# Optimization experiments

Hardware: AMD Instinct MI355X
Metric: run time of the kernel (lower is better)

## Reference

```python
import jax, jax.numpy as jnp
import numpy as np
from jax import lax

HID = 768          # hidden_dim / embedding_dim
IN = 64            # input_dim = max_seq_length // num_heads
SEQ = 512          # max_seq_length
GROUPS = IN        # conv groups
BLUR_K = 5
BLUR_SIGMA = 1.0


def _gauss1d(k, sigma):
    half = (k - 1) * 0.5
    x = np.linspace(-half, half, k)
    pdf = np.exp(-0.5 * (x / sigma) ** 2)
    return pdf / pdf.sum()


def setup_inputs() -> dict:
    key = jax.random.key(0)
    ks = jax.random.split(key, 8)
    s = 0.02
    return {
        "inputs": jax.random.normal(ks[0], (16, SEQ, HID), jnp.float32),
        # Conv1d(768, 768, k=3, groups=64): weight [out_ch, in_ch/groups, k]
        "conv_w": jax.random.normal(ks[1], (HID, HID // GROUPS, 3), jnp.float32) * s,
        "conv_b": jnp.zeros((HID,), jnp.float32),
        "ln_g": jnp.ones((IN,), jnp.float32),
        "ln_b": jnp.zeros((IN,), jnp.float32),
        # function_info: Linear(64, 64), torch weight convention [out, in]
        "fi_w": jax.random.normal(ks[2], (IN, IN), jnp.float32) * s,
        "fi_b": jnp.zeros((IN,), jnp.float32),
        # block_info: Linear(64, 1)
        "bi_w": jax.random.normal(ks[3], (1, IN), jnp.float32) * s,
        "bi_b": jnp.zeros((1,), jnp.float32),
    }


def _forward(inputs, conv_w, conv_b, ln_g, ln_b, fi_w, fi_b, bi_w, bi_b):
    x = inputs.reshape(-1, HID, IN)  # [Bn, 768, 64] (raw row-major view, as torch .view)
    q = k = v = m = x

    # q: grouped Conv1d + residual, GELU, LayerNorm over last dim (64)
    qc = lax.conv_general_dilated(
        q, conv_w, window_strides=(1,), padding=[(1, 1)],
        feature_group_count=GROUPS, dimension_numbers=("NCH", "OIH", "NCH"))
    qc = qc + conv_b[None, :, None]
    q = jax.nn.gelu(qc + q, approximate=False)
    mu = jnp.mean(q, axis=-1, keepdims=True)
    var = jnp.mean(jnp.square(q - mu), axis=-1, keepdims=True)
    q = (q - mu) * lax.rsqrt(var + 1e-5) * ln_g + ln_b

    # v: Linear(64,64) + GELU
    v = jax.nn.gelu(v @ fi_w.T + fi_b, approximate=False)

    # k: dropout (eval -> identity), softmax over dim=-2 (channel axis), GELU
    k = jax.nn.gelu(jax.nn.softmax(k, axis=-2), approximate=False)

    # m: GaussianBlur(5, sigma fixed 1.0) over (H=768, W=64) with reflect pad, then Linear(64,1)
    g = _gauss1d(BLUR_K, BLUR_SIGMA)
    kern = jnp.asarray(np.outer(g, g), m.dtype)[None, None]  # [1,1,5,5]
    p = BLUR_K // 2
    mp = jnp.pad(m[:, None], ((0, 0), (0, 0), (p, p), (p, p)), mode="reflect")
    m = lax.conv_general_dilated(
        mp, kern, (1, 1), "VALID", dimension_numbers=("NCHW", "OIHW", "NCHW"))[:, 0]
    m = m @ bi_w.T + bi_b                        # [Bn, 768, 1]
    mask = jnp.broadcast_to(m, (m.shape[0], HID, HID))  # expand to [Bn,768,768]

    # SDPA: scale = 1/sqrt(E) with E = q.shape[-1] = 64; additive float mask
    scores = jnp.einsum("bce,bde->bcd", q, k) * (1.0 / np.sqrt(IN)) + mask
    attn = jax.nn.softmax(scores, axis=-1)
    out = jnp.einsum("bcd,bde->bce", attn, v)    # [Bn, 768, 64]
    return out.reshape(-1, SEQ, HID)


def reference(inputs, conv_w, conv_b, ln_g, ln_b, fi_w, fi_b, bi_w, bi_b):
    return _forward(inputs, conv_w, conv_b, ln_g, ln_b, fi_w, fi_b, bi_w, bi_b)
```

## Files before the change

### kernel.cpp

```cpp
#include <hip/hip_runtime.h>
#include <hip/hip_bf16.h>
#include <math.h>

#define NB 128
#define NC 768
#define NE 64
#define IPG 12

typedef __hip_bfloat16 bf16;
typedef __bf16 bf16v8 __attribute__((ext_vector_type(8)));
typedef __bf16 bf16v4 __attribute__((ext_vector_type(4)));
typedef __bf16 bf16v2 __attribute__((ext_vector_type(2)));
typedef float f32x4 __attribute__((ext_vector_type(4)));
typedef unsigned int u32;
typedef u32 u32x4 __attribute__((ext_vector_type(4)));

__device__ __forceinline__ float gelu_exact(float x) {
    float ax = fabsf(x);
    float t = __builtin_amdgcn_rcpf(fmaf(0.2316419f, ax, 1.0f));
    float poly = t * fmaf(t, fmaf(t, fmaf(t, fmaf(t, 1.330274429f,
                  -1.821255978f), 1.781477937f), -0.356563782f), 0.319381530f);
    float pdf = 0.3989422804f * __expf(-0.5f * ax * ax);
    float c = fmaf(-pdf, poly, 1.0f);
    float cdf = (x >= 0.f) ? c : 1.0f - c;
    return x * cdf;
}

#define MFMA16(a, b, c) __builtin_amdgcn_mfma_f32_16x16x32_bf16(a, b, c, 0, 0, 0)

__device__ __forceinline__ void gload_lds16(const void* g, void* l) {
    __builtin_amdgcn_global_load_lds(
        (const __attribute__((address_space(1))) void*)g,
        (__attribute__((address_space(3))) void*)l, 16, 0, 0);
}

__global__ __launch_bounds__(256) void k_conv(
    const float* __restrict__ x, const float* __restrict__ cw,
    const float* __restrict__ cb, const float* __restrict__ lg,
    const float* __restrict__ lb, bf16* __restrict__ qo,
    float* __restrict__ sp)
{
    int b = blockIdx.x >> 4;
    int chunk = blockIdx.x & 15;
    int w = threadIdx.x >> 6;
    int g = __builtin_amdgcn_readfirstlane(chunk * 4 + w);
    int h = threadIdx.x & 63;
    const float* xb = x + ((size_t)b * NC + g * IPG) * NE;

    float xi[IPG], xm[IPG], xp[IPG];
    #pragma unroll
    for (int i = 0; i < IPG; ++i) {
        xi[i] = xb[i * NE + h];
        float up = __shfl_up(xi[i], 1);
        float dn = __shfl_down(xi[i], 1);
        xm[i] = h ? up : 0.f;
        xp[i] = (h < 63) ? dn : 0.f;
    }

    float es = 0.f;
    #pragma unroll
    for (int i = 0; i < IPG; ++i) es += __expf(xi[i]);
    __shared__ float red[4][64];
    red[w][h] = es;
    __syncthreads();
    if (w == 0) {
        float s = red[0][h] + red[1][h] + red[2][h] + red[3][h];
        sp[(size_t)(b * 16 + chunk) * 64 + h] = s;
    }

    float gam = lg[h], bet = lb[h];
    const float* wg = cw + (size_t)g * IPG * 36;

    for (int o = 0; o < IPG; ++o) {
        const float* wo = wg + o * 36;
        float acc = cb[g * IPG + o];
        #pragma unroll
        for (int i = 0; i < IPG; ++i)
            acc = fmaf(xm[i], wo[i*3], fmaf(xi[i], wo[i*3+1], fmaf(xp[i], wo[i*3+2], acc)));
        float gl = gelu_exact(acc + xi[o]);
        float s1 = gl, s2 = gl * gl;
        #pragma unroll
        for (int off = 32; off; off >>= 1) {
            s1 += __shfl_xor(s1, off);
            s2 += __shfl_xor(s2, off);
        }
        float mu  = s1 * (1.f / 64.f);
        float var = s2 * (1.f / 64.f) - mu * mu;
        float qn = (gl - mu) * rsqrtf(var + 1e-5f) * gam + bet;
        qo[((size_t)b * NC + g * IPG + o) * NE + h] = __float2bfloat16(qn * 0.125f);
    }
}

__global__ __launch_bounds__(256) void k_vk(
    const float* __restrict__ x, const float* __restrict__ fw,
    const float* __restrict__ fb, const float* __restrict__ sp,
    bf16* __restrict__ ko, bf16* __restrict__ vTo)
{
    int chunk = blockIdx.x, b = blockIdx.y;
    int tid = threadIdx.x, w = tid >> 6, l = tid & 63;
    int lr = l & 15, lc = (l >> 4) * 8;
    int rowb = chunk * 64 + w * 16;
    const float* xb = x + (size_t)b * NC * NE;

    __shared__ float sts[64];
    if (tid < 64) {
        float s = 0.f;
        #pragma unroll
        for (int p = 0; p < 16; ++p) s += sp[(size_t)(b * 16 + p) * 64 + tid];
        sts[tid] = 1.f / s;
    }

    bf16v8 bfr[4][2];
    float fbias[4];
    #pragma unroll
    for (int nt = 0; nt < 4; ++nt) {
        #pragma unroll
        for (int kt = 0; kt < 2; ++kt) {
            const float* p = fw + (nt*16 + lr) * 64 + kt*32 + lc;
            bf16v8 t;
            #pragma unroll
            for (int j = 0; j < 8; ++j) t[j] = (__bf16)p[j];
            bfr[nt][kt] = t;
        }
        fbias[nt] = fb[nt*16 + lr];
    }
    __syncthreads();

    float isA[8], isB[8];
    #pragma unroll
    for (int j = 0; j < 8; ++j) { isA[j] = sts[lc + j]; isB[j] = sts[32 + lc + j]; }

    const float* pa = xb + (size_t)(rowb + lr) * NE;
    float xa[8], xc[8];
    #pragma unroll
    for (int j = 0; j < 8; ++j) xa[j] = pa[lc + j];
    #pragma unroll
    for (int j = 0; j < 8; ++j) xc[j] = pa[32 + lc + j];

    bf16v8 a0, a1;
    #pragma unroll
    for (int j = 0; j < 8; ++j) a0[j] = (__bf16)xa[j];
    #pragma unroll
    for (int j = 0; j < 8; ++j) a1[j] = (__bf16)xc[j];

    bf16v8 kv0, kv1;
    #pragma unroll
    for (int j = 0; j < 8; ++j) kv0[j] = (__bf16)gelu_exact(__expf(xa[j]) * isA[j]);
    #pragma unroll
    for (int j = 0; j < 8; ++j) kv1[j] = (__bf16)gelu_exact(__expf(xc[j]) * isB[j]);
    bf16* kp = ko + ((size_t)b * NC + rowb + lr) * NE + lc;
    *(bf16v8*)kp = kv0;
    *(bf16v8*)(kp + 32) = kv1;

    #pragma unroll
    for (int nt = 0; nt < 4; ++nt) {
        f32x4 acc = {fbias[nt], fbias[nt], fbias[nt], fbias[nt]};
        acc = MFMA16(a0, bfr[nt][0], acc);
        acc = MFMA16(a1, bfr[nt][1], acc);
        bf16v4 pk;
        #pragma unroll
        for (int r = 0; r < 4; ++r) pk[r] = (__bf16)gelu_exact(acc[r]);
        int c = rowb + (l >> 4) * 4;
        *(bf16v4*)&vTo[((size_t)b * NE + nt*16 + lr) * NC + c] = pk;
    }
}

__device__ __forceinline__ bf16v8 softmax_exch(f32x4 s0, f32x4 s1, float& rsum,
                                               int srcA, int srcB, int hq) {
    float p0 = __expf(s0[0]), p1 = __expf(s0[1]), p2 = __expf(s0[2]), p3 = __expf(s0[3]);
    float p4 = __expf(s1[0]), p5 = __expf(s1[1]), p6 = __expf(s1[2]), p7 = __expf(s1[3]);
    rsum += ((p0 + p1) + (p2 + p3)) + ((p4 + p5) + (p6 + p7));
    bf16v2 t0; t0[0] = (__bf16)p0; t0[1] = (__bf16)p1;
    bf16v2 t1; t1[0] = (__bf16)p2; t1[1] = (__bf16)p3;
    bf16v2 t2; t2[0] = (__bf16)p4; t2[1] = (__bf16)p5;
    bf16v2 t3; t3[0] = (__bf16)p6; t3[1] = (__bf16)p7;
    u32 w0 = __builtin_bit_cast(u32, t0), w1 = __builtin_bit_cast(u32, t1);
    u32 w2 = __builtin_bit_cast(u32, t2), w3 = __builtin_bit_cast(u32, t3);
    u32 c0A = (u32)__shfl((int)w0, srcA), c1A = (u32)__shfl((int)w1, srcA);
    u32 c2A = (u32)__shfl((int)w2, srcA), c3A = (u32)__shfl((int)w3, srcA);
    u32 c0B = (u32)__shfl((int)w0, srcB), c1B = (u32)__shfl((int)w1, srcB);
    u32 c2B = (u32)__shfl((int)w2, srcB), c3B = (u32)__shfl((int)w3, srcB);
    u32x4 pau = { hq ? c2A : c0A, hq ? c3A : c1A,
                  hq ? c2B : c0B, hq ? c3B : c1B };
    return __builtin_bit_cast(bf16v8, pau);
}

__global__ __launch_bounds__(256, 3) void k_attn(const bf16* __restrict__ qb,
                                                 const bf16* __restrict__ kb,
                                                 const bf16* __restrict__ vT,
                                                 float* __restrict__ out) {
    __shared__ __align__(16) __bf16 ldsK[2][4096];
    __shared__ __align__(16) __bf16 ldsV[2][4096];

    int bid = blockIdx.x;
    int swz = (bid & 7) * 96 + (bid >> 3);
    int b = swz / 6, qt = swz - b * 6;
    int w = threadIdx.x >> 6, l = threadIdx.x & 63;
    int q0 = qt * 128 + w * 32;
    int lr = l & 15, hi = l >> 4;
    int hq = hi >> 1;
    int srcA = lr + ((hi & 1) << 5);
    int srcB = srcA + 16;

    int krow_ = w * 8 + (l >> 3);
    int kc16_ = (l & 7) ^ (l >> 3);
    const char* kgbase = (const char*)(kb + (size_t)b * NC * NE)
                       + krow_ * 128 + kc16_ * 16;
    int ve_   = w * 16 + (l >> 2);
    int vc16_ = (l & 3) ^ ((l >> 3) & 3);
    const char* vgbase = (const char*)(vT + (size_t)b * NE * NC)
                       + ve_ * 1536 + vc16_ * 16;

    int krd0 = lr * 64 + ((hi ^ (lr & 7)) << 3);
    int krd1 = lr * 64 + (((4 + hi) ^ (lr & 7)) << 3);
    int vsel = (lr >> 1) & 3;
    int vrd  = lr * 32 + ((hi ^ vsel) << 3);

    const bf16* qp = qb + ((size_t)b * NC + q0 + lr) * NE + hi * 8;
    bf16v8 qf00 = *(const bf16v8*)qp;
    bf16v8 qf01 = *(const bf16v8*)(qp + 32);
    bf16v8 qf10 = *(const bf16v8*)(qp + 16 * NE);
    bf16v8 qf11 = *(const bf16v8*)(qp + 16 * NE + 32);

    f32x4 o00 = {0,0,0,0}, o01 = {0,0,0,0}, o02 = {0,0,0,0}, o03 = {0,0,0,0};
    f32x4 o10 = {0,0,0,0}, o11 = {0,0,0,0}, o12 = {0,0,0,0}, o13 = {0,0,0,0};
    float rsum0 = 0.f, rsum1 = 0.f;

    gload_lds16(kgbase,           &ldsK[0][w * 512]);
    gload_lds16(kgbase + 4096,    &ldsK[0][2048 + w * 512]);
    gload_lds16(vgbase,           &ldsV[0][w * 512]);
    gload_lds16(vgbase + 64,      &ldsV[0][2048 + w * 512]);
    __syncthreads();

    int cur = 0;
    for (int ph = 0; ph < 12; ++ph) {
        if (ph < 11) {
            const char* kg = kgbase + (size_t)(2 * ph + 2) * 4096;
            gload_lds16(kg,        &ldsK[cur ^ 1][w * 512]);
            gload_lds16(kg + 4096, &ldsK[cur ^ 1][2048 + w * 512]);
            const char* vg = vgbase + (size_t)(2 * ph + 2) * 64;
            gload_lds16(vg,        &ldsV[cur ^ 1][w * 512]);
            gload_lds16(vg + 64,   &ldsV[cur ^ 1][2048 + w * 512]);
        }

        #pragma unroll
        for (int sub = 0; sub < 2; ++sub) {
            const __bf16* Kc = &ldsK[cur][sub * 2048];
            const __bf16* Vc = &ldsV[cur][sub * 2048];
            bf16v8 ka0 = *(const bf16v8*)&Kc[krd0];
            bf16v8 ka1 = *(const bf16v8*)&Kc[krd1];
            bf16v8 ka2 = *(const bf16v8*)&Kc[krd0 + 1024];
            bf16v8 ka3 = *(const bf16v8*)&Kc[krd1 + 1024];
            bf16v8 v0  = *(const bf16v8*)&Vc[vrd];
            bf16v8 v1  = *(const bf16v8*)&Vc[vrd + 512];
            bf16v8 v2  = *(const bf16v8*)&Vc[vrd + 1024];
            bf16v8 v3  = *(const bf16v8*)&Vc[vrd + 1536];

            __builtin_amdgcn_s_setprio(1);
            f32x4 s00 = {0,0,0,0}, s01 = {0,0,0,0};
            s00 = MFMA16(ka0, qf00, s00);
            s00 = MFMA16(ka1, qf01, s00);
            s01 = MFMA16(ka2, qf00, s01);
            s01 = MFMA16(ka3, qf01, s01);
            f32x4 s10 = {0,0,0,0}, s11 = {0,0,0,0};
            s10 = MFMA16(ka0, qf10, s10);
            s10 = MFMA16(ka1, qf11, s10);
            s11 = MFMA16(ka2, qf10, s11);
            s11 = MFMA16(ka3, qf11, s11);
            __builtin_amdgcn_s_setprio(0);

            bf16v8 pa0 = softmax_exch(s00, s01, rsum0, srcA, srcB, hq);
            bf16v8 pa1 = softmax_exch(s10, s11, rsum1, srcA, srcB, hq);

            __builtin_amdgcn_s_setprio(1);
            o00 = MFMA16(pa0, v0, o00);
            o01 = MFMA16(pa0, v1, o01);
            o02 = MFMA16(pa0, v2, o02);
            o03 = MFMA16(pa0, v3, o03);
            o10 = MFMA16(pa1, v0, o10);
            o11 = MFMA16(pa1, v1, o11);
            o12 = MFMA16(pa1, v2, o12);
            o13 = MFMA16(pa1, v3, o13);
            __builtin_amdgcn_s_setprio(0);
        }

        __syncthreads();
        cur ^= 1;
    }

    rsum0 += __shfl_xor(rsum0, 16);
    rsum0 += __shfl_xor(rsum0, 32);
    rsum1 += __shfl_xor(rsum1, 16);
    rsum1 += __shfl_xor(rsum1, 32);
    float inv0 = 1.f / rsum0, inv1 = 1.f / rsum1;

    int qrow0 = q0 + hi * 4;
    #pragma unroll
    for (int r = 0; r < 4; ++r) {
        float iq = __shfl(inv0, hi * 4 + r);
        float* op = out + ((size_t)b * NC + qrow0 + r) * NE + lr;
        op[0]  = o00[r] * iq;
        op[16] = o01[r] * iq;
        op[32] = o02[r] * iq;
        op[48] = o03[r] * iq;
    }
    int qrow1 = q0 + 16 + hi * 4;
    #pragma unroll
    for (int r = 0; r < 4; ++r) {
        float iq = __shfl(inv1, hi * 4 + r);
        float* op = out + ((size_t)b * NC + qrow1 + r) * NE + lr;
        op[0]  = o10[r] * iq;
        op[16] = o11[r] * iq;
        op[32] = o12[r] * iq;
        op[48] = o13[r] * iq;
    }
}

extern "C" void kernel_launch(void* const* d_in, const int* in_sizes, int n_in,
                              void* d_out, int out_size, void* d_ws, size_t ws_size,
                              hipStream_t stream) {
    (void)in_sizes; (void)n_in; (void)out_size; (void)ws_size;
    const float* x      = (const float*)d_in[0];
    const float* conv_w = (const float*)d_in[1];
    const float* conv_b = (const float*)d_in[2];
    const float* ln_g   = (const float*)d_in[3];
    const float* ln_b   = (const float*)d_in[4];
    const float* fi_w   = (const float*)d_in[5];
    const float* fi_b   = (const float*)d_in[6];

    bf16* qbuf = (bf16*)d_ws;
    bf16* kbuf = qbuf + (size_t)NB * NC * NE;
    bf16* vT   = kbuf + (size_t)NB * NC * NE;
    float* stats = (float*)(vT + (size_t)NB * NC * NE);
    float* out = (float*)d_out;

    k_conv<<<dim3(NB * 16), 256, 0, stream>>>(x, conv_w, conv_b, ln_g, ln_b,
                                              qbuf, stats);
    k_vk<<<dim3(12, NB), 256, 0, stream>>>(x, fi_w, fi_b, stats, kbuf, vT);
    k_attn<<<dim3(768), 256, 0, stream>>>(qbuf, kbuf, vT, out);
}
```

Baseline: 78.89 us.

## Switch attention to 32x32x16 MFMA tiles with exp2-based softmax

Rewrites the attention inner loop to use 32x32x16 bf16 MFMAs instead of 16x16x32, so each wave computes a 32-query by 32-key score tile in one accumulator and produces 32x32 output tiles. The softmax now uses exp2f, with log2(e) folded into the Q scale in the conv kernel, and the P-to-A-fragment exchange becomes a single xor-32 shuffle. The output is transposed and written as vectorized f32x4 stores, and the final row-sum reduction needs only one shuffle. This is meant to cut shuffle, exp and instruction overhead per tile, at the cost of larger accumulator register pressure and new LDS read patterns that must stay bank-conflict free.

```diff
diff --git a/kernel.cpp b/kernel.cpp
--- a/kernel.cpp
+++ b/kernel.cpp
@@ -6,12 +6,15 @@
 #define NC 768
 #define NE 64
 #define IPG 12
+
+#define QSCALE 0.18033688011112042f
 
 typedef __hip_bfloat16 bf16;
 typedef __bf16 bf16v8 __attribute__((ext_vector_type(8)));
 typedef __bf16 bf16v4 __attribute__((ext_vector_type(4)));
 typedef __bf16 bf16v2 __attribute__((ext_vector_type(2)));
 typedef float f32x4 __attribute__((ext_vector_type(4)));
+typedef float f32x16 __attribute__((ext_vector_type(16)));
 typedef unsigned int u32;
 typedef u32 u32x4 __attribute__((ext_vector_type(4)));
 
@@ -27,11 +30,17 @@
 }
 
 #define MFMA16(a, b, c) __builtin_amdgcn_mfma_f32_16x16x32_bf16(a, b, c, 0, 0, 0)
+#define MFMA32(a, b, c) __builtin_amdgcn_mfma_f32_32x32x16_bf16(a, b, c, 0, 0, 0)
 
 __device__ __forceinline__ void gload_lds16(const void* g, void* l) {
     __builtin_amdgcn_global_load_lds(
         (const __attribute__((address_space(1))) void*)g,
         (__attribute__((address_space(3))) void*)l, 16, 0, 0);
+}
+
+__device__ __forceinline__ u32 pkbf(float a, float b) {
+    bf16v2 t; t[0] = (__bf16)a; t[1] = (__bf16)b;
+    return __builtin_bit_cast(u32, t);
 }
 
 __global__ __launch_bounds__(256) void k_conv(
@@ -87,7 +96,7 @@
         float mu  = s1 * (1.f / 64.f);
         float var = s2 * (1.f / 64.f) - mu * mu;
         float qn = (gl - mu) * rsqrtf(var + 1e-5f) * gam + bet;
-        qo[((size_t)b * NC + g * IPG + o) * NE + h] = __float2bfloat16(qn * 0.125f);
+        qo[((size_t)b * NC + g * IPG + o) * NE + h] = __float2bfloat16(qn * QSCALE);
     }
 }
 
@@ -165,26 +174,6 @@
     }
 }
 
-__device__ __forceinline__ bf16v8 softmax_exch(f32x4 s0, f32x4 s1, float& rsum,
-                                               int srcA, int srcB, int hq) {
-    float p0 = __expf(s0[0]), p1 = __expf(s0[1]), p2 = __expf(s0[2]), p3 = __expf(s0[3]);
-    float p4 = __expf(s1[0]), p5 = __expf(s1[1]), p6 = __expf(s1[2]), p7 = __expf(s1[3]);
-    rsum += ((p0 + p1) + (p2 + p3)) + ((p4 + p5) + (p6 + p7));
-    bf16v2 t0; t0[0] = (__bf16)p0; t0[1] = (__bf16)p1;
-    bf16v2 t1; t1[0] = (__bf16)p2; t1[1] = (__bf16)p3;
-    bf16v2 t2; t2[0] = (__bf16)p4; t2[1] = (__bf16)p5;
-    bf16v2 t3; t3[0] = (__bf16)p6; t3[1] = (__bf16)p7;
-    u32 w0 = __builtin_bit_cast(u32, t0), w1 = __builtin_bit_cast(u32, t1);
-    u32 w2 = __builtin_bit_cast(u32, t2), w3 = __builtin_bit_cast(u32, t3);
-    u32 c0A = (u32)__shfl((int)w0, srcA), c1A = (u32)__shfl((int)w1, srcA);
-    u32 c2A = (u32)__shfl((int)w2, srcA), c3A = (u32)__shfl((int)w3, srcA);
-    u32 c0B = (u32)__shfl((int)w0, srcB), c1B = (u32)__shfl((int)w1, srcB);
-    u32 c2B = (u32)__shfl((int)w2, srcB), c3B = (u32)__shfl((int)w3, srcB);
-    u32x4 pau = { hq ? c2A : c0A, hq ? c3A : c1A,
-                  hq ? c2B : c0B, hq ? c3B : c1B };
-    return __builtin_bit_cast(bf16v8, pau);
-}
-
 __global__ __launch_bounds__(256, 3) void k_attn(const bf16* __restrict__ qb,
                                                  const bf16* __restrict__ kb,
                                                  const bf16* __restrict__ vT,
@@ -197,10 +186,7 @@
     int b = swz / 6, qt = swz - b * 6;
     int w = threadIdx.x >> 6, l = threadIdx.x & 63;
     int q0 = qt * 128 + w * 32;
-    int lr = l & 15, hi = l >> 4;
-    int hq = hi >> 1;
-    int srcA = lr + ((hi & 1) << 5);
-    int srcB = srcA + 16;
+    int l31 = l & 31, b5 = l >> 5;
 
     int krow_ = w * 8 + (l >> 3);
     int kc16_ = (l & 7) ^ (l >> 3);
@@ -211,25 +197,30 @@
     const char* vgbase = (const char*)(vT + (size_t)b * NE * NC)
                        + ve_ * 1536 + vc16_ * 16;
 
-    int krd0 = lr * 64 + ((hi ^ (lr & 7)) << 3);
-    int krd1 = lr * 64 + (((4 + hi) ^ (lr & 7)) << 3);
-    int vsel = (lr >> 1) & 3;
-    int vrd  = lr * 32 + ((hi ^ vsel) << 3);
-
-    const bf16* qp = qb + ((size_t)b * NC + q0 + lr) * NE + hi * 8;
-    bf16v8 qf00 = *(const bf16v8*)qp;
-    bf16v8 qf01 = *(const bf16v8*)(qp + 32);
-    bf16v8 qf10 = *(const bf16v8*)(qp + 16 * NE);
-    bf16v8 qf11 = *(const bf16v8*)(qp + 16 * NE + 32);
-
-    f32x4 o00 = {0,0,0,0}, o01 = {0,0,0,0}, o02 = {0,0,0,0}, o03 = {0,0,0,0};
-    f32x4 o10 = {0,0,0,0}, o11 = {0,0,0,0}, o12 = {0,0,0,0}, o13 = {0,0,0,0};
-    float rsum0 = 0.f, rsum1 = 0.f;
-
-    gload_lds16(kgbase,           &ldsK[0][w * 512]);
-    gload_lds16(kgbase + 4096,    &ldsK[0][2048 + w * 512]);
-    gload_lds16(vgbase,           &ldsV[0][w * 512]);
-    gload_lds16(vgbase + 64,      &ldsV[0][2048 + w * 512]);
+    int krd[4];
+    #pragma unroll
+    for (int c = 0; c < 4; ++c)
+        krd[c] = l31 * 64 + ((((c << 1) | b5) ^ (l & 7)) << 3);
+    int vsw = (l31 >> 1) & 3;
+    int vrd[2];
+    #pragma unroll
+    for (int ck = 0; ck < 2; ++ck)
+        vrd[ck] = l31 * 32 + ((((ck << 1) | b5) ^ vsw) << 3);
+
+    const bf16* qp = qb + ((size_t)b * NC + q0 + l31) * NE + b5 * 8;
+    bf16v8 qf0 = *(const bf16v8*)qp;
+    bf16v8 qf1 = *(const bf16v8*)(qp + 16);
+    bf16v8 qf2 = *(const bf16v8*)(qp + 32);
+    bf16v8 qf3 = *(const bf16v8*)(qp + 48);
+
+    f32x16 o0 = {0,0,0,0,0,0,0,0,0,0,0,0,0,0,0,0};
+    f32x16 o1 = {0,0,0,0,0,0,0,0,0,0,0,0,0,0,0,0};
+    float rsum = 0.f;
+
+    gload_lds16(kgbase,        &ldsK[0][w * 512]);
+    gload_lds16(kgbase + 4096, &ldsK[0][2048 + w * 512]);
+    gload_lds16(vgbase,        &ldsV[0][w * 512]);
+    gload_lds16(vgbase + 64,   &ldsV[0][2048 + w * 512]);
     __syncthreads();
 
     int cur = 0;
@@ -247,72 +238,68 @@
         for (int sub = 0; sub < 2; ++sub) {
             const __bf16* Kc = &ldsK[cur][sub * 2048];
             const __bf16* Vc = &ldsV[cur][sub * 2048];
-            bf16v8 ka0 = *(const bf16v8*)&Kc[krd0];
-            bf16v8 ka1 = *(const bf16v8*)&Kc[krd1];
-            bf16v8 ka2 = *(const bf16v8*)&Kc[krd0 + 1024];
-            bf16v8 ka3 = *(const bf16v8*)&Kc[krd1 + 1024];
-            bf16v8 v0  = *(const bf16v8*)&Vc[vrd];
-            bf16v8 v1  = *(const bf16v8*)&Vc[vrd + 512];
-            bf16v8 v2  = *(const bf16v8*)&Vc[vrd + 1024];
-            bf16v8 v3  = *(const bf16v8*)&Vc[vrd + 1536];
-
+
+            bf16v8 ka0 = *(const bf16v8*)&Kc[krd[0]];
+            bf16v8 ka1 = *(const bf16v8*)&Kc[krd[1]];
+            bf16v8 ka2 = *(const bf16v8*)&Kc[krd[2]];
+            bf16v8 ka3 = *(const bf16v8*)&Kc[krd[3]];
             __builtin_amdgcn_s_setprio(1);
-            f32x4 s00 = {0,0,0,0}, s01 = {0,0,0,0};
-            s00 = MFMA16(ka0, qf00, s00);
-            s00 = MFMA16(ka1, qf01, s00);
-            s01 = MFMA16(ka2, qf00, s01);
-            s01 = MFMA16(ka3, qf01, s01);
-            f32x4 s10 = {0,0,0,0}, s11 = {0,0,0,0};
-            s10 = MFMA16(ka0, qf10, s10);
-            s10 = MFMA16(ka1, qf11, s10);
-            s11 = MFMA16(ka2, qf10, s11);
-            s11 = MFMA16(ka3, qf11, s11);
+            f32x16 s = {0,0,0,0,0,0,0,0,0,0,0,0,0,0,0,0};
+            s = MFMA32(ka0, qf0, s);
+            s = MFMA32(ka1, qf1, s);
+            s = MFMA32(ka2, qf2, s);
+            s = MFMA32(ka3, qf3, s);
             __builtin_amdgcn_s_setprio(0);
 
-            bf16v8 pa0 = softmax_exch(s00, s01, rsum0, srcA, srcB, hq);
-            bf16v8 pa1 = softmax_exch(s10, s11, rsum1, srcA, srcB, hq);
-
-            __builtin_amdgcn_s_setprio(1);
-            o00 = MFMA16(pa0, v0, o00);
-            o01 = MFMA16(pa0, v1, o01);
-            o02 = MFMA16(pa0, v2, o02);
-            o03 = MFMA16(pa0, v3, o03);
-            o10 = MFMA16(pa1, v0, o10);
-            o11 = MFMA16(pa1, v1, o11);
-            o12 = MFMA16(pa1, v2, o12);
-            o13 = MFMA16(pa1, v3, o13);
-            __builtin_amdgcn_s_setprio(0);
+            u32 wv[8];
+            #pragma unroll
+            for (int qd = 0; qd < 4; ++qd) {
+                float a0 = exp2f(s[4*qd + 0]);
+                float a1 = exp2f(s[4*qd + 1]);
+                float a2 = exp2f(s[4*qd + 2]);
+                float a3 = exp2f(s[4*qd + 3]);
+                rsum += (a0 + a1) + (a2 + a3);
+                wv[2*qd]     = pkbf(a0, a1);
+                wv[2*qd + 1] = pkbf(a2, a3);
+            }
+
+            #pragma unroll
+            for (int ck = 0; ck < 2; ++ck) {
+                u32 y1 = (u32)__shfl_xor((int)(b5 ? wv[4*ck]     : wv[4*ck+2]), 32);
+                u32 y2 = (u32)__shfl_xor((int)(b5 ? wv[4*ck + 1] : wv[4*ck+3]), 32);
+                u32x4 fw_;
+                fw_[0] = b5 ? y1 : wv[4*ck];
+                fw_[1] = b5 ? y2 : wv[4*ck + 1];
+                fw_[2] = b5 ? wv[4*ck + 2] : y1;
+                fw_[3] = b5 ? wv[4*ck + 3] : y2;
+                bf16v8 pf = __builtin_bit_cast(bf16v8, fw_);
+                bf16v8 va0 = *(const bf16v8*)&Vc[vrd[ck]];
+                bf16v8 va1 = *(const bf16v8*)&Vc[vrd[ck] + 1024];
+                __builtin_amdgcn_s_setprio(1);
+                o0 = MFMA32(va0, pf, o0);
+                o1 = MFMA32(va1, pf, o1);
+                __builtin_amdgcn_s_setprio(0);
+            }
         }
 
         __syncthreads();
         cur ^= 1;
     }
 
-    rsum0 += __shfl_xor(rsum0, 16);
-    rsum0 += __shfl_xor(rsum0, 32);
-    rsum1 += __shfl_xor(rsum1, 16);
-    rsum1 += __shfl_xor(rsum1, 32);
-    float inv0 = 1.f / rsum0, inv1 = 1.f / rsum1;
-
-    int qrow0 = q0 + hi * 4;
-    #pragma unroll
-    for (int r = 0; r < 4; ++r) {
-        float iq = __shfl(inv0, hi * 4 + r);
-        float* op = out + ((size_t)b * NC + qrow0 + r) * NE + lr;
-        op[0]  = o00[r] * iq;
-        op[16] = o01[r] * iq;
-        op[32] = o02[r] * iq;
-        op[48] = o03[r] * iq;
-    }
-    int qrow1 = q0 + 16 + hi * 4;
-    #pragma unroll
-    for (int r = 0; r < 4; ++r) {
-        float iq = __shfl(inv1, hi * 4 + r);
-        float* op = out + ((size_t)b * NC + qrow1 + r) * NE + lr;
-        op[0]  = o10[r] * iq;
-        op[16] = o11[r] * iq;
-        op[32] = o12[r] * iq;
-        op[48] = o13[r] * iq;
+    rsum += __shfl_xor(rsum, 32);
+    float inv = 1.f / rsum;
+
+    float* ob = out + ((size_t)b * NC + q0 + l31) * NE + b5 * 4;
+    #pragma unroll
+    for (int qd = 0; qd < 4; ++qd) {
+        f32x4 v0, v1;
+        #pragma unroll
+        for (int r = 0; r < 4; ++r) {
+            v0[r] = o0[4*qd + r] * inv;
+            v1[r] = o1[4*qd + r] * inv;
+        }
+        *(f32x4*)&ob[qd * 8]      = v0;
+        *(f32x4*)&ob[32 + qd * 8] = v1;
     }
 }
 
```

New measurement: 82.80 us. 5.0% more time.
